# Optimization experiments

Hardware: AMD Instinct MI355X
Metric: run time of the kernel (lower is better)

## Reference

```python
import jax, jax.numpy as jnp
import numpy as np

D_MODEL, D_FF, N_EXPERTS, TOP_K = 1024, 4096, 4, 2
B, S = 4, 2048


def setup_inputs() -> dict:
    key = jax.random.key(0)
    ks = jax.random.split(key, 7)
    s_r = 1.0 / np.sqrt(D_MODEL)
    s_f = 1.0 / np.sqrt(D_FF)
    return {
        "x": jax.random.normal(ks[0], (B, S, D_MODEL), dtype=jnp.float32),
        "Wr": jax.random.uniform(ks[1], (D_MODEL, N_EXPERTS), jnp.float32, -s_r, s_r),
        "br": jnp.zeros((N_EXPERTS,), jnp.float32),
        "W1": jax.random.uniform(ks[2], (N_EXPERTS, D_MODEL, D_FF), jnp.float32, -s_r, s_r),
        "b1": jax.random.uniform(ks[3], (N_EXPERTS, D_FF), jnp.float32, -s_r, s_r),
        "W2": jax.random.uniform(ks[4], (N_EXPERTS, D_FF, D_MODEL), jnp.float32, -s_f, s_f),
        "b2": jax.random.uniform(ks[5], (N_EXPERTS, D_MODEL), jnp.float32, -s_f, s_f),
    }


def reference(x, Wr, br, W1, b1, W2, b2):
    # Router: (B,S,E)
    router_logits = jnp.einsum("bsd,de->bse", x, Wr) + br
    router_probs = jax.nn.softmax(router_logits, axis=-1)
    top_k_probs, top_k_idx = jax.lax.top_k(router_probs, TOP_K)  # (B,S,K)
    top_k_probs = top_k_probs / jnp.sum(top_k_probs, axis=-1, keepdims=True)

    # Dense all-experts compute (faithful to original module).
    h = jnp.einsum("bsd,edf->bsef", x, W1) + b1          # (B,S,E,F)
    h = jax.nn.gelu(h, approximate=False)                 # torch nn.GELU (erf)
    expert_out = jnp.einsum("bsef,efd->bsed", h, W2) + b2  # (B,S,E,D)

    # Gather top-k expert outputs and combine with renormalized probs.
    sel = jnp.take_along_axis(expert_out, top_k_idx[..., None], axis=2)  # (B,S,K,D)
    out = jnp.sum(sel * top_k_probs[..., None], axis=2)   # (B,S,D)
    return out
```

## Files before the change

### kernel.cpp

```cpp
#include <hip/hip_runtime.h>
#include <hip/hip_bf16.h>
#include <hip/hip_fp16.h>
#include <stdint.h>

typedef float    f32x4 __attribute__((ext_vector_type(4)));
typedef float    fvec4 __attribute__((ext_vector_type(4)));
typedef _Float16 f16x8 __attribute__((ext_vector_type(8)));
typedef _Float16 f16x4 __attribute__((ext_vector_type(4)));

#define D_MODEL 1024
#define D_FF    4096
#define NTOK    8192
#define CAP_ROWS 16896
#define NRB      132

#define OFF_W1  0UL
#define OFF_W2  33554432UL
#define OFF_XG  67108864UL
#define OFF_H   101711872UL
#define OFF_CNT 240123904UL
#define OFF_OFS 240123936UL
#define OFF_TOK 240124160UL
#define OFF_E12 240259328UL
#define OFF_W12 240292096UL
#define WS_NEED 240357632UL

__device__ __forceinline__ void gload_lds16(const void* g, void* l) {
  __builtin_amdgcn_global_load_lds(
      (const __attribute__((address_space(1))) unsigned int*)g,
      (__attribute__((address_space(3))) unsigned int*)l, 16, 0, 0);
}

__device__ __forceinline__ float fast_gelu(float v) {
  float v2 = v * v;
  float y2 = v * (2.302118131f + 0.10293924f * v2);
  float t = exp2f(y2);
  return v - v * __builtin_amdgcn_rcpf(1.f + t);
}

__device__ __forceinline__ void wtrans_body(
    const float* __restrict__ in, _Float16* __restrict__ out,
    int K, int N, int e, int n0, int k0, float (*tile)[65]) {
  const float* src = in + (size_t)e * K * N;
  _Float16* dst = out + (size_t)e * K * N;
  int t = threadIdx.x;
  {
    int kk = t >> 2, nc = (t & 3) * 16;
    const float* p = src + (size_t)(k0 + kk) * N + n0 + nc;
#pragma unroll
    for (int j = 0; j < 4; ++j) {
      fvec4 v = *(const fvec4*)(p + j * 4);
      tile[kk][nc + j * 4 + 0] = v[0]; tile[kk][nc + j * 4 + 1] = v[1];
      tile[kk][nc + j * 4 + 2] = v[2]; tile[kk][nc + j * 4 + 3] = v[3];
    }
  }
  __syncthreads();
  {
    int nn = t >> 2, kb = (t & 3) * 16;
    f16x8 o0, o1;
#pragma unroll
    for (int j = 0; j < 8; ++j) o0[j] = (_Float16)tile[kb + j][nn];
#pragma unroll
    for (int j = 0; j < 8; ++j) o1[j] = (_Float16)tile[kb + 8 + j][nn];
    _Float16* q = dst + (size_t)(n0 + nn) * K + k0 + kb;
    *(f16x8*)q = o0;
    *((f16x8*)q + 1) = o1;
  }
}

__global__ __launch_bounds__(256) void rwc_k(
    const float* __restrict__ x, const float* __restrict__ Wr,
    const float* __restrict__ br, int* __restrict__ e12,
    float* __restrict__ w12,
    const float* __restrict__ W1, _Float16* __restrict__ W1f,
    _Float16* __restrict__ x16) {
  __shared__ float tile[64][65];
  int b = blockIdx.x;
  if (b >= 2048) {
    int bb = b - 2048;
    int n0 = (bb & 63) * 64, k0 = ((bb >> 6) & 15) * 64, e = bb >> 10;
    wtrans_body(W1, W1f, 1024, 4096, e, n0, k0, tile);
    return;
  }
  int wid = threadIdx.x >> 6, lane = threadIdx.x & 63;
  int t = b * 4 + wid;
  const float* xr = x + (size_t)t * D_MODEL;
  _Float16* xw = x16 + (size_t)t * D_MODEL;
  float a0 = 0.f, a1 = 0.f, a2 = 0.f, a3 = 0.f;
#pragma unroll
  for (int c = 0; c < 4; ++c) {
    int d0 = c * 256 + lane * 4;
    fvec4 xv = *(const fvec4*)(xr + d0);
    f16x4 o = {(_Float16)xv[0], (_Float16)xv[1], (_Float16)xv[2], (_Float16)xv[3]};
    *(f16x4*)(xw + d0) = o;
#pragma unroll
    for (int j = 0; j < 4; ++j) {
      fvec4 wv = *(const fvec4*)(Wr + (size_t)(d0 + j) * 4);
      a0 += xv[j] * wv[0]; a1 += xv[j] * wv[1];
      a2 += xv[j] * wv[2]; a3 += xv[j] * wv[3];
    }
  }
#pragma unroll
  for (int m = 32; m; m >>= 1) {
    a0 += __shfl_xor(a0, m, 64); a1 += __shfl_xor(a1, m, 64);
    a2 += __shfl_xor(a2, m, 64); a3 += __shfl_xor(a3, m, 64);
  }
  if (lane == 0) {
    float l[4] = {a0 + br[0], a1 + br[1], a2 + br[2], a3 + br[3]};
    int e1 = 0; float m1 = l[0];
#pragma unroll
    for (int e = 1; e < 4; ++e) if (l[e] > m1) { m1 = l[e]; e1 = e; }
    int e2 = -1; float m2 = -1e30f;
#pragma unroll
    for (int e = 0; e < 4; ++e) if (e != e1 && l[e] > m2) { m2 = l[e]; e2 = e; }
    float tt = expf(m2 - m1);
    float w1 = 1.f / (1.f + tt), w2 = tt / (1.f + tt);
    e12[t] = e1 | (e2 << 8);
    w12[2 * t] = w1; w12[2 * t + 1] = w2;
  }
}

__global__ __launch_bounds__(256) void plan_k(
    int* __restrict__ e12, const float* __restrict__ w12,
    int* __restrict__ counts, int* __restrict__ offs,
    int* __restrict__ tok) {
  __shared__ int ls[4][256];
  __shared__ int lt[4];
  __shared__ int lo[5];
  int tid = threadIdx.x;
  int t0 = tid * 32;
  int pe[32];
  int c0 = 0, c1 = 0, c2 = 0, c3 = 0;
#pragma unroll
  for (int j = 0; j < 32; ++j) {
    int p = e12[t0 + j];
    pe[j] = p;
    int e1 = p & 255, e2 = p >> 8;
    c0 += (e1 == 0) + (e2 == 0);
    c1 += (e1 == 1) + (e2 == 1);
    c2 += (e1 == 2) + (e2 == 2);
    c3 += (e1 == 3) + (e2 == 3);
  }
  ls[0][tid] = c0; ls[1][tid] = c1; ls[2][tid] = c2; ls[3][tid] = c3;
  __syncthreads();
  int wv = tid >> 6, lane = tid & 63;
  {
    int s0 = ls[wv][lane * 4 + 0], s1 = ls[wv][lane * 4 + 1];
    int s2 = ls[wv][lane * 4 + 2], s3 = ls[wv][lane * 4 + 3];
    int s = s0 + s1 + s2 + s3;
    int incl = s;
#pragma unroll
    for (int d = 1; d < 64; d <<= 1) {
      int tsh = __shfl_up(incl, d, 64);
      if (lane >= d) incl += tsh;
    }
    int excl = incl - s;
    ls[wv][lane * 4 + 0] = excl;
    ls[wv][lane * 4 + 1] = excl + s0;
    ls[wv][lane * 4 + 2] = excl + s0 + s1;
    ls[wv][lane * 4 + 3] = excl + s0 + s1 + s2;
    if (lane == 63) lt[wv] = incl;
  }
  __syncthreads();
  if (tid == 0) {
    int o = 0;
#pragma unroll
    for (int e = 0; e < 4; ++e) {
      lo[e] = o; offs[e] = o; counts[e] = lt[e];
      o += (lt[e] + 127) & ~127;
    }
    lo[4] = o; offs[4] = o;
  }
  __syncthreads();
  int b0 = lo[0] + ls[0][tid], b1 = lo[1] + ls[1][tid];
  int b2 = lo[2] + ls[2][tid], b3 = lo[3] + ls[3][tid];
#pragma unroll
  for (int j = 0; j < 32; ++j) {
    int p = pe[j];
    int t = t0 + j;
    int e1 = p & 255, e2 = p >> 8;
    int s1 = (e1 == 0) ? b0 : (e1 == 1) ? b1 : (e1 == 2) ? b2 : b3;
    tok[s1] = t;
    b0 += (e1 == 0); b1 += (e1 == 1); b2 += (e1 == 2); b3 += (e1 == 3);
    int s2 = (e2 == 0) ? b0 : (e2 == 1) ? b1 : (e2 == 2) ? b2 : b3;
    tok[s2] = t;
    b0 += (e2 == 0); b1 += (e2 == 1); b2 += (e2 == 2); b3 += (e2 == 3);
    e12[t] = s1 | (s2 << 16);
  }
#pragma unroll
  for (int e = 0; e < 4; ++e) {
    int start = lo[e] + lt[e];
    int end = lo[e + 1];
    for (int i = start + tid; i < end; i += 256) tok[i] = 0;
  }
}

__device__ __forceinline__ f16x8 lds_frag(const char* base, int row, int kbyte) {
  return *(const f16x8*)(base + row * 128 + (kbyte ^ ((row & 7) << 4)));
}

#define GVM8   asm volatile("s_waitcnt vmcnt(8)" ::: "memory")
#define GVM0   asm volatile("s_waitcnt vmcnt(0)" ::: "memory")
#define GBAR   asm volatile("s_barrier" ::: "memory")
#define GLGKM  asm volatile("s_waitcnt lgkmcnt(0)" ::: "memory")

__global__ __launch_bounds__(256, 2) void gemm1x_k(
    const _Float16* __restrict__ x16, const _Float16* __restrict__ B,
    const float* __restrict__ bias, const int* __restrict__ offs,
    const int* __restrict__ counts, const int* __restrict__ tok,
    _Float16* __restrict__ outH,
    const float* __restrict__ W2, _Float16* __restrict__ W2f) {
  __shared__ char lds[49152];
  int bid = blockIdx.x;
  if (bid >= 2112) {
    int bb = bid - 2112;
    int n0 = (bb & 15) * 64, k0 = ((bb >> 4) & 63) * 64, e = bb >> 10;
    wtrans_body(W2, W2f, 4096, 1024, e, n0, k0, (float(*)[65])lds);
    return;
  }
  int wg = (bid & 7) * 264 + (bid >> 3);
  int col = wg & 15, row = wg >> 4;
  int rowBase = row * 128;
  if (rowBase >= offs[4]) return;
  int e = 0;
  while (e < 3 && rowBase >= offs[e + 1]) ++e;
  if (rowBase >= offs[e] + counts[e]) return;
  int colBase = col * 256;

  int tid = threadIdx.x, wid = tid >> 6, lane = tid & 63;
  int wr = wid >> 1, wc = wid & 1;
  int ln = lane & 15;
  int srow = lane >> 3;
  int kx = (lane & 7) ^ srow;
  const _Float16* Asrc[4];
#pragma unroll
  for (int i = 0; i < 4; ++i) {
    int tk = tok[rowBase + (wid * 4 + i) * 8 + srow];
    Asrc[i] = x16 + (size_t)tk * 1024 + kx * 8;
  }
  const _Float16* Bbase = B + (size_t)e * D_FF * 1024 + (size_t)colBase * 1024 + kx * 8;
  char* ldsA = lds;
  char* ldsB = lds + 16384;

  f32x4 acc[4][8];
  f32x4 zero = {0.f, 0.f, 0.f, 0.f};
#pragma unroll
  for (int m = 0; m < 4; ++m)
#pragma unroll
    for (int n = 0; n < 8; ++n) acc[m][n] = zero;

  for (int k0 = 0; k0 < 1024; k0 += 64) {
#pragma unroll
    for (int i = 0; i < 4; ++i) {
      int chunk = wid * 4 + i;
      gload_lds16(Asrc[i] + k0, ldsA + chunk * 1024);
    }
#pragma unroll
    for (int i = 0; i < 8; ++i) {
      int chunk = wid * 8 + i;
      gload_lds16(Bbase + (size_t)(chunk * 8 + srow) * 1024 + k0, ldsB + chunk * 1024);
    }
    __syncthreads();
#pragma unroll
    for (int kk = 0; kk < 2; ++kk) {
      int kbyte = kk * 64 + (lane >> 4) * 16;
      f16x8 af[4], bf[8];
#pragma unroll
      for (int m = 0; m < 4; ++m)
        af[m] = lds_frag(ldsA, wr * 64 + m * 16 + ln, kbyte);
#pragma unroll
      for (int n = 0; n < 8; ++n)
        bf[n] = lds_frag(ldsB, wc * 128 + n * 16 + ln, kbyte);
#pragma unroll
      for (int m = 0; m < 4; ++m)
#pragma unroll
        for (int n = 0; n < 8; ++n)
          acc[m][n] = __builtin_amdgcn_mfma_f32_16x16x32_f16(af[m], bf[n], acc[m][n], 0, 0, 0);
    }
    __syncthreads();
  }

  int col0 = colBase + wc * 128 + ln;
  float bv[8];
#pragma unroll
  for (int n = 0; n < 8; ++n) bv[n] = bias[(size_t)e * D_FF + col0 + n * 16];
#pragma unroll
  for (int m = 0; m < 4; ++m) {
    int rbase = rowBase + wr * 64 + m * 16 + (lane >> 4) * 4;
#pragma unroll
    for (int j = 0; j < 4; ++j) {
      size_t ro = (size_t)(rbase + j) * D_FF;
#pragma unroll
      for (int n = 0; n < 8; ++n) {
        float v = fast_gelu(acc[m][n][j] + bv[n]);
        outH[ro + col0 + n * 16] = (_Float16)v;
      }
    }
  }
}

__global__ __launch_bounds__(256, 2) void gemm2_k(
    const _Float16* __restrict__ A, const _Float16* __restrict__ B,
    const float* __restrict__ bias, const int* __restrict__ offs,
    const int* __restrict__ counts, _Float16* __restrict__ Eout) {
  __shared__ char lds[65536];
  int bid = blockIdx.x;
  int wg = (bid & 7) * 132 + (bid >> 3);
  int col = wg & 7, row = wg >> 3;
  int rowBase = row * 128;
  if (rowBase >= offs[4]) return;
  int e = 0;
  while (e < 3 && rowBase >= offs[e + 1]) ++e;
  int eoff = offs[e], cnt = counts[e];
  if (rowBase >= eoff + cnt) return;
  int colBase = col * 128;

  int tid = threadIdx.x, wid = tid >> 6, lane = tid & 63;
  int wr = wid >> 1, wc = wid & 1;
  int ln = lane & 15;
  int srow = lane >> 3;
  int kx = (lane & 7) ^ srow;
  const _Float16* Abase = A + (size_t)rowBase * 4096 + kx * 8;
  const _Float16* Bbase = B + (size_t)e * D_MODEL * 4096 + (size_t)colBase * 4096 + kx * 8;

  f32x4 acc[4][4];
  f32x4 zero = {0.f, 0.f, 0.f, 0.f};
#pragma unroll
  for (int m = 0; m < 4; ++m)
#pragma unroll
    for (int n = 0; n < 4; ++n) acc[m][n] = zero;

  auto STAGE = [&](int kt, int b) {
    char* lA = lds + (b << 15);
    char* lB = lA + 16384;
    int k0 = kt * 64;
#pragma unroll
    for (int i = 0; i < 4; ++i) {
      int chunk = wid * 4 + i;
      gload_lds16(Abase + (size_t)(chunk * 8 + srow) * 4096 + k0, lA + chunk * 1024);
      gload_lds16(Bbase + (size_t)(chunk * 8 + srow) * 4096 + k0, lB + chunk * 1024);
    }
  };

  STAGE(0, 0);
  STAGE(1, 1);

  for (int t = 0; t < 64; ++t) {
    GVM8;
    GBAR;
    const char* cA = lds + ((t & 1) << 15);
    const char* cB = cA + 16384;
#pragma unroll
    for (int kk = 0; kk < 2; ++kk) {
      int kbyte = kk * 64 + (lane >> 4) * 16;
      f16x8 af[4], bf[4];
#pragma unroll
      for (int m = 0; m < 4; ++m)
        af[m] = lds_frag(cA, wr * 64 + m * 16 + ln, kbyte);
#pragma unroll
      for (int n = 0; n < 4; ++n)
        bf[n] = lds_frag(cB, wc * 64 + n * 16 + ln, kbyte);
      GLGKM;
      __builtin_amdgcn_s_setprio(1);
#pragma unroll
      for (int m = 0; m < 4; ++m)
#pragma unroll
        for (int n = 0; n < 4; ++n)
          acc[m][n] = __builtin_amdgcn_mfma_f32_16x16x32_f16(af[m], bf[n], acc[m][n], 0, 0, 0);
      __builtin_amdgcn_s_setprio(0);
    }
    GBAR;
    int tn = t + 2; if (tn > 63) tn = 63;
    STAGE(tn, t & 1);
  }
  GVM0;

  int col0 = colBase + wc * 64 + ln;
  float bv[4];
#pragma unroll
  for (int n = 0; n < 4; ++n) bv[n] = bias[(size_t)e * D_MODEL + col0 + n * 16];
#pragma unroll
  for (int m = 0; m < 4; ++m) {
    int rbase = rowBase + wr * 64 + m * 16 + (lane >> 4) * 4;
#pragma unroll
    for (int j = 0; j < 4; ++j) {
      int grow = rbase + j;
      if (grow - eoff < cnt) {
        size_t o = (size_t)grow * D_MODEL + col0;
#pragma unroll
        for (int n = 0; n < 4; ++n)
          Eout[o + n * 16] = (_Float16)(acc[m][n][j] + bv[n]);
      }
    }
  }
}

__global__ __launch_bounds__(256) void combine_k(
    const _Float16* __restrict__ Eout, const int* __restrict__ sl12,
    const float* __restrict__ w12, float* __restrict__ out) {
  int t = blockIdx.x * 2 + (threadIdx.x >> 7);
  int tid = threadIdx.x & 127;
  int p = sl12[t];
  int s1 = p & 0xffff, s2 = (p >> 16) & 0xffff;
  float w1 = w12[2 * t], w2 = w12[2 * t + 1];
  f16x8 a = *(const f16x8*)(Eout + (size_t)s1 * D_MODEL + tid * 8);
  f16x8 b = *(const f16x8*)(Eout + (size_t)s2 * D_MODEL + tid * 8);
  fvec4 o0, o1;
#pragma unroll
  for (int j = 0; j < 4; ++j) {
    o0[j] = w1 * (float)a[j] + w2 * (float)b[j];
    o1[j] = w1 * (float)a[4 + j] + w2 * (float)b[4 + j];
  }
  float* dst = out + (size_t)t * D_MODEL + tid * 8;
  *(fvec4*)dst = o0;
  *(fvec4*)(dst + 4) = o1;
}

extern "C" void kernel_launch(void* const* d_in, const int* in_sizes, int n_in,
                              void* d_out, int out_size, void* d_ws, size_t ws_size,
                              hipStream_t stream) {
  const float* x  = (const float*)d_in[0];
  const float* Wr = (const float*)d_in[1];
  const float* br = (const float*)d_in[2];
  const float* W1 = (const float*)d_in[3];
  const float* b1 = (const float*)d_in[4];
  const float* W2 = (const float*)d_in[5];
  const float* b2 = (const float*)d_in[6];
  float* out = (float*)d_out;
  char* ws = (char*)d_ws;
  if (ws_size < WS_NEED) return;

  _Float16* W1f = (_Float16*)(ws + OFF_W1);
  _Float16* W2f = (_Float16*)(ws + OFF_W2);
  _Float16* x16 = (_Float16*)(ws + OFF_XG);
  _Float16* H   = (_Float16*)(ws + OFF_H);
  int*   counts = (int*)(ws + OFF_CNT);
  int*   offs   = (int*)(ws + OFF_OFS);
  int*   tok    = (int*)(ws + OFF_TOK);
  int*   e12    = (int*)(ws + OFF_E12);
  float* w12    = (float*)(ws + OFF_W12);
  _Float16* Eout = x16;

  rwc_k<<<6144, 256, 0, stream>>>(x, Wr, br, e12, w12, W1, W1f, x16);
  plan_k<<<1, 256, 0, stream>>>(e12, w12, counts, offs, tok);
  gemm1x_k<<<6208, 256, 0, stream>>>(x16, W1f, b1, offs, counts, tok, H, W2, W2f);
  gemm2_k<<<NRB * 8, 256, 0, stream>>>(H, W2f, b2, offs, counts, Eout);
  combine_k<<<NTOK / 2, 256, 0, stream>>>(Eout, e12, w12, out);
}
```

Baseline: 434.4 us.

## Enlarge gemm2 tiles to 256x256 with 8 waves and quadrant-pipelined LDS staging

The second expert GEMM moves from 128x128 tiles with 4 waves to 256x256 tiles with 8 waves. It uses 128KB of dynamic LDS split into A and B half-tiles, and the next k-slices are streamed in per quadrant while MFMAs run on the current one. Expert row padding goes from 128 to 256 to match, so gemm1 grid counts and workspace offsets change too. The aim is higher arithmetic intensity and less global traffic per FLOP, at the cost of one block per CU, more padding rows, and many barriers per k-step.

```diff
diff --git a/kernel.cpp b/kernel.cpp
--- a/kernel.cpp
+++ b/kernel.cpp
@@ -11,19 +11,20 @@
 #define D_MODEL 1024
 #define D_FF    4096
 #define NTOK    8192
-#define CAP_ROWS 16896
-#define NRB      132
-
-#define OFF_W1  0UL
-#define OFF_W2  33554432UL
-#define OFF_XG  67108864UL
-#define OFF_H   101711872UL
-#define OFF_CNT 240123904UL
-#define OFF_OFS 240123936UL
-#define OFF_TOK 240124160UL
-#define OFF_E12 240259328UL
-#define OFF_W12 240292096UL
-#define WS_NEED 240357632UL
+#define CAP_ROWS 17408
+#define RB1      136
+#define RB2      68
+
+#define OFF_W2  0UL
+#define OFF_X16 33554432UL
+#define OFF_W1  50331648UL
+#define OFF_H   83886080UL
+#define OFF_CNT 226492416UL
+#define OFF_OFS 226492448UL
+#define OFF_TOK 226492480UL
+#define OFF_E12 226562112UL
+#define OFF_W12 226594880UL
+#define WS_NEED 226660416UL
 
 __device__ __forceinline__ void gload_lds16(const void* g, void* l) {
   __builtin_amdgcn_global_load_lds(
@@ -167,7 +168,7 @@
 #pragma unroll
     for (int e = 0; e < 4; ++e) {
       lo[e] = o; offs[e] = o; counts[e] = lt[e];
-      o += (lt[e] + 127) & ~127;
+      o += (lt[e] + 255) & ~255;
     }
     lo[4] = o; offs[4] = o;
   }
@@ -199,8 +200,9 @@
   return *(const f16x8*)(base + row * 128 + (kbyte ^ ((row & 7) << 4)));
 }
 
-#define GVM8   asm volatile("s_waitcnt vmcnt(8)" ::: "memory")
 #define GVM0   asm volatile("s_waitcnt vmcnt(0)" ::: "memory")
+#define GVM6   asm volatile("s_waitcnt vmcnt(6)" ::: "memory")
+#define GLG8   asm volatile("s_waitcnt lgkmcnt(8)" ::: "memory")
 #define GBAR   asm volatile("s_barrier" ::: "memory")
 #define GLGKM  asm volatile("s_waitcnt lgkmcnt(0)" ::: "memory")
 
@@ -212,13 +214,13 @@
     const float* __restrict__ W2, _Float16* __restrict__ W2f) {
   __shared__ char lds[49152];
   int bid = blockIdx.x;
-  if (bid >= 2112) {
-    int bb = bid - 2112;
+  if (bid >= 2176) {
+    int bb = bid - 2176;
     int n0 = (bb & 15) * 64, k0 = ((bb >> 4) & 63) * 64, e = bb >> 10;
     wtrans_body(W2, W2f, 4096, 1024, e, n0, k0, (float(*)[65])lds);
     return;
   }
-  int wg = (bid & 7) * 264 + (bid >> 3);
+  int wg = (bid & 7) * 272 + (bid >> 3);
   int col = wg & 15, row = wg >> 4;
   int rowBase = row * 128;
   if (rowBase >= offs[4]) return;
@@ -299,100 +301,169 @@
   }
 }
 
-__global__ __launch_bounds__(256, 2) void gemm2_k(
+#define STG_A(h, k0, dst)                                                     \
+  _Pragma("unroll") for (int j = 0; j < 2; ++j) {                             \
+    int chunk = wid * 2 + j;                                                  \
+    gload_lds16(Ag + (size_t)((h)*128 + chunk * 8 + srow) * 4096 + (k0),      \
+                (dst) + chunk * 1024);                                        \
+  }
+#define STG_B(q, k0, dst)                                                     \
+  _Pragma("unroll") for (int j = 0; j < 2; ++j) {                             \
+    int chunk = wid * 2 + j;                                                  \
+    gload_lds16(Bg + (size_t)((q)*128 + chunk * 8 + srow) * 4096 + (k0),      \
+                (dst) + chunk * 1024);                                        \
+  }
+#define RDA8(base)                                                            \
+  _Pragma("unroll") for (int m = 0; m < 4; ++m)                               \
+  _Pragma("unroll") for (int kk = 0; kk < 2; ++kk)                            \
+      af[m*2 + kk] = lds_frag((base), wr*64 + m*16 + ln, kk*64 + kq);
+#define RDB4(dst, base)                                                       \
+  _Pragma("unroll") for (int n = 0; n < 2; ++n)                               \
+  _Pragma("unroll") for (int kk = 0; kk < 2; ++kk)                            \
+      dst[n*2 + kk] = lds_frag((base), wc*32 + n*16 + ln, kk*64 + kq);
+#define QUAD(h, q, bfr)                                                       \
+  __builtin_amdgcn_s_setprio(1);                                              \
+  _Pragma("unroll") for (int m = 0; m < 4; ++m)                               \
+  _Pragma("unroll") for (int n = 0; n < 2; ++n)                               \
+  _Pragma("unroll") for (int kk = 0; kk < 2; ++kk)                            \
+      acc[(h)*4 + m][(q)*2 + n] = __builtin_amdgcn_mfma_f32_16x16x32_f16(     \
+          af[m*2 + kk], bfr[n*2 + kk], acc[(h)*4 + m][(q)*2 + n], 0, 0, 0);   \
+  __builtin_amdgcn_s_setprio(0);
+
+__global__ __launch_bounds__(512) void gemm2_k(
     const _Float16* __restrict__ A, const _Float16* __restrict__ B,
     const float* __restrict__ bias, const int* __restrict__ offs,
     const int* __restrict__ counts, _Float16* __restrict__ Eout) {
-  __shared__ char lds[65536];
+  extern __shared__ char smem[];
   int bid = blockIdx.x;
-  int wg = (bid & 7) * 132 + (bid >> 3);
-  int col = wg & 7, row = wg >> 3;
-  int rowBase = row * 128;
+  int wg = (bid & 7) * 34 + (bid >> 3);
+  int col = wg & 3, row = wg >> 2;
+  int rowBase = row * 256;
   if (rowBase >= offs[4]) return;
   int e = 0;
   while (e < 3 && rowBase >= offs[e + 1]) ++e;
   int eoff = offs[e], cnt = counts[e];
   if (rowBase >= eoff + cnt) return;
-  int colBase = col * 128;
+  int colBase = col * 256;
 
   int tid = threadIdx.x, wid = tid >> 6, lane = tid & 63;
-  int wr = wid >> 1, wc = wid & 1;
-  int ln = lane & 15;
+  int wr = wid >> 2, wc = wid & 3;
+  int ln = lane & 15, kq = (lane >> 4) * 16;
   int srow = lane >> 3;
   int kx = (lane & 7) ^ srow;
-  const _Float16* Abase = A + (size_t)rowBase * 4096 + kx * 8;
-  const _Float16* Bbase = B + (size_t)e * D_MODEL * 4096 + (size_t)colBase * 4096 + kx * 8;
-
-  f32x4 acc[4][4];
+
+  const _Float16* Ag = A + (size_t)rowBase * 4096 + kx * 8;
+  const _Float16* Bg = B + (size_t)e * D_MODEL * 4096 + (size_t)colBase * 4096 + kx * 8;
+
+  char* A00 = smem;
+  char* A01 = smem + 16384;
+  char* A10 = smem + 32768;
+  char* A11 = smem + 49152;
+  char* B00 = smem + 65536;
+  char* B01 = smem + 81920;
+  char* B10 = smem + 98304;
+  char* B11 = smem + 114688;
+
+  f32x4 acc[8][4];
   f32x4 zero = {0.f, 0.f, 0.f, 0.f};
 #pragma unroll
-  for (int m = 0; m < 4; ++m)
-#pragma unroll
-    for (int n = 0; n < 4; ++n) acc[m][n] = zero;
-
-  auto STAGE = [&](int kt, int b) {
-    char* lA = lds + (b << 15);
-    char* lB = lA + 16384;
-    int k0 = kt * 64;
-#pragma unroll
-    for (int i = 0; i < 4; ++i) {
-      int chunk = wid * 4 + i;
-      gload_lds16(Abase + (size_t)(chunk * 8 + srow) * 4096 + k0, lA + chunk * 1024);
-      gload_lds16(Bbase + (size_t)(chunk * 8 + srow) * 4096 + k0, lB + chunk * 1024);
-    }
-  };
-
-  STAGE(0, 0);
-  STAGE(1, 1);
-
-  for (int t = 0; t < 64; ++t) {
-    GVM8;
-    GBAR;
-    const char* cA = lds + ((t & 1) << 15);
-    const char* cB = cA + 16384;
-#pragma unroll
-    for (int kk = 0; kk < 2; ++kk) {
-      int kbyte = kk * 64 + (lane >> 4) * 16;
-      f16x8 af[4], bf[4];
-#pragma unroll
-      for (int m = 0; m < 4; ++m)
-        af[m] = lds_frag(cA, wr * 64 + m * 16 + ln, kbyte);
-#pragma unroll
-      for (int n = 0; n < 4; ++n)
-        bf[n] = lds_frag(cB, wc * 64 + n * 16 + ln, kbyte);
-      GLGKM;
-      __builtin_amdgcn_s_setprio(1);
-#pragma unroll
-      for (int m = 0; m < 4; ++m)
-#pragma unroll
-        for (int n = 0; n < 4; ++n)
-          acc[m][n] = __builtin_amdgcn_mfma_f32_16x16x32_f16(af[m], bf[n], acc[m][n], 0, 0, 0);
-      __builtin_amdgcn_s_setprio(0);
-    }
-    GBAR;
-    int tn = t + 2; if (tn > 63) tn = 63;
-    STAGE(tn, t & 1);
+  for (int i = 0; i < 8; ++i)
+#pragma unroll
+    for (int jn = 0; jn < 4; ++jn) acc[i][jn] = zero;
+
+  STG_A(0, 0, A00);
+  STG_B(0, 0, B00);
+  STG_B(1, 0, B01);
+  STG_A(1, 0, A01);
+  STG_A(0, 64, A10);
+  STG_B(0, 64, B10);
+  STG_B(1, 64, B11);
+  GVM6;
+  GBAR;
+
+  f16x8 af[8], bf0[4], bf1[4];
+
+  for (int it = 0; it < 32; ++it) {
+    int k1 = (2 * it + 1) * 64;
+    int kt2 = 2 * it + 2; if (kt2 > 63) kt2 = 63;
+    int kt3 = 2 * it + 3; if (kt3 > 63) kt3 = 63;
+    int k2 = kt2 * 64, k3 = kt3 * 64;
+
+    RDA8(A00); RDB4(bf0, B00);
+    STG_A(1, k1, A11);
+    GLG8; GBAR; GLGKM;
+    QUAD(0, 0, bf0);
+    GBAR;
+
+    RDB4(bf1, B01);
+    STG_A(0, k2, A00);
+    GBAR; GLGKM;
+    QUAD(0, 1, bf1);
+    GBAR;
+
+    RDA8(A01);
+    STG_B(0, k2, B00);
+    GBAR; GLGKM;
+    QUAD(1, 0, bf0);
+    GBAR;
+
+    STG_B(1, k2, B01);
+    GBAR; GLGKM;
+    QUAD(1, 1, bf1);
+    GVM6;
+    GBAR;
+
+    RDA8(A10); RDB4(bf0, B10);
+    STG_A(1, k2, A01);
+    GLG8; GBAR; GLGKM;
+    QUAD(0, 0, bf0);
+    GBAR;
+
+    RDB4(bf1, B11);
+    STG_A(0, k3, A10);
+    GBAR; GLGKM;
+    QUAD(0, 1, bf1);
+    GBAR;
+
+    RDA8(A11);
+    STG_B(0, k3, B10);
+    GBAR; GLGKM;
+    QUAD(1, 0, bf0);
+    GBAR;
+
+    STG_B(1, k3, B11);
+    GBAR; GLGKM;
+    QUAD(1, 1, bf1);
+    GVM6;
+    GBAR;
   }
   GVM0;
 
-  int col0 = colBase + wc * 64 + ln;
   float bv[4];
 #pragma unroll
-  for (int n = 0; n < 4; ++n) bv[n] = bias[(size_t)e * D_MODEL + col0 + n * 16];
-#pragma unroll
-  for (int m = 0; m < 4; ++m) {
-    int rbase = rowBase + wr * 64 + m * 16 + (lane >> 4) * 4;
-#pragma unroll
-    for (int j = 0; j < 4; ++j) {
-      int grow = rbase + j;
-      if (grow - eoff < cnt) {
-        size_t o = (size_t)grow * D_MODEL + col0;
-#pragma unroll
-        for (int n = 0; n < 4; ++n)
-          Eout[o + n * 16] = (_Float16)(acc[m][n][j] + bv[n]);
+  for (int q = 0; q < 2; ++q)
+#pragma unroll
+    for (int n = 0; n < 2; ++n)
+      bv[q*2 + n] = bias[(size_t)e * D_MODEL + colBase + q*128 + wc*32 + n*16 + ln];
+#pragma unroll
+  for (int h = 0; h < 2; ++h)
+#pragma unroll
+    for (int m = 0; m < 4; ++m) {
+      int rbase = rowBase + h*128 + wr*64 + m*16 + (lane >> 4) * 4;
+#pragma unroll
+      for (int j = 0; j < 4; ++j) {
+        int grow = rbase + j;
+        if (grow - eoff < cnt) {
+          size_t o = (size_t)grow * D_MODEL + colBase;
+#pragma unroll
+          for (int q = 0; q < 2; ++q)
+#pragma unroll
+            for (int n = 0; n < 2; ++n)
+              Eout[o + q*128 + wc*32 + n*16 + ln] =
+                  (_Float16)(acc[h*4 + m][q*2 + n][j] + bv[q*2 + n]);
+        }
       }
     }
-  }
 }
 
 __global__ __launch_bounds__(256) void combine_k(
@@ -430,9 +501,9 @@
   char* ws = (char*)d_ws;
   if (ws_size < WS_NEED) return;
 
+  _Float16* W2f = (_Float16*)(ws + OFF_W2);
+  _Float16* x16 = (_Float16*)(ws + OFF_X16);
   _Float16* W1f = (_Float16*)(ws + OFF_W1);
-  _Float16* W2f = (_Float16*)(ws + OFF_W2);
-  _Float16* x16 = (_Float16*)(ws + OFF_XG);
   _Float16* H   = (_Float16*)(ws + OFF_H);
   int*   counts = (int*)(ws + OFF_CNT);
   int*   offs   = (int*)(ws + OFF_OFS);
@@ -441,9 +512,12 @@
   float* w12    = (float*)(ws + OFF_W12);
   _Float16* Eout = x16;
 
+  hipFuncSetAttribute((const void*)gemm2_k,
+                      hipFuncAttributeMaxDynamicSharedMemorySize, 131072);
+
   rwc_k<<<6144, 256, 0, stream>>>(x, Wr, br, e12, w12, W1, W1f, x16);
   plan_k<<<1, 256, 0, stream>>>(e12, w12, counts, offs, tok);
-  gemm1x_k<<<6208, 256, 0, stream>>>(x16, W1f, b1, offs, counts, tok, H, W2, W2f);
-  gemm2_k<<<NRB * 8, 256, 0, stream>>>(H, W2f, b2, offs, counts, Eout);
+  gemm1x_k<<<6272, 256, 0, stream>>>(x16, W1f, b1, offs, counts, tok, H, W2, W2f);
+  gemm2_k<<<RB2 * 4, 512, 131072, stream>>>(H, W2f, b2, offs, counts, Eout);
   combine_k<<<NTOK / 2, 256, 0, stream>>>(Eout, e12, w12, out);
 }
```

New measurement: 480.9 us. 10.7% more time.
